# Performance work log

Measured on AMD Instinct MI355X. Metric: run time of the kernel, lower is better.

The kernel has to match this reference:

```python
import jax, jax.numpy as jnp
import numpy as np

B, P, NTIME, NLATENT, NSPATIAL = 4, 2, 16, 32, 2048


def sqrt_act(x):
    # signed square root: sign(x) * sqrt(|x|) (odd, monotone activation used in ERA5_PredRNN)
    return jnp.sign(x) * jnp.sqrt(jnp.abs(x))


def setup_inputs() -> dict:
    key = jax.random.key(0)
    ks = jax.random.split(key, 10)
    T, C, X = NTIME, NLATENT, NSPATIAL
    # xavier-uniform bounds (torch fan_in = T*C, fan_out = T*C for (t,T,c); T,T for 2D)
    s3 = (6.0 / (T * C + T * C)) ** 0.5
    s2 = (6.0 / (T + T)) ** 0.5
    x = jax.random.normal(ks[0], (B, P, T, C, X), jnp.float32)
    K0 = jax.random.uniform(ks[1], (T, T, C), jnp.float32, -s3, s3)
    Q0 = jax.random.uniform(ks[2], (T, T, C), jnp.float32, -s3, s3)
    V0 = jax.random.uniform(ks[3], (T, T, C), jnp.float32, -s3, s3)
    K1 = jax.random.uniform(ks[4], (T, T), jnp.float32, -s2, s2)
    Q1 = jax.random.uniform(ks[5], (T, T), jnp.float32, -s2, s2)
    V1 = jax.random.uniform(ks[6], (T, T), jnp.float32, -s2, s2)

    def ortho3(kk):
        # mimics nn.init.orthogonal_ on (T,T,T): rows (flattened to T x T*T) are orthonormal
        m = jax.random.normal(kk, (T * T, T), jnp.float32)
        q, _ = jnp.linalg.qr(m)  # (T*T, T), orthonormal columns
        return q.T.reshape(T, T, T)

    enc = ortho3(ks[7])
    dec = ortho3(ks[8])
    a = jnp.ones((T, X), jnp.float32)
    w = jnp.ones((T, X), jnp.float32) / (X * T)
    return dict(x=x, K0=K0, Q0=Q0, V0=V0, K1=K1, Q1=Q1, V1=V1,
                enc=enc, dec=dec, a=a, w=w)


def reference(x, K0, Q0, V0, K1, Q1, V1, enc, dec, a, w):
    # --- layer 0: per-latent-channel time mixing (tTc) ---
    k = jnp.einsum('tTc,bpTcx->bptcx', K0, x)
    q0 = jnp.einsum('tTc,bpTcx->bptcx', Q0, x)
    v = jnp.einsum('tTc,bpTcx->bptcx', V0, x)
    h = sqrt_act(jnp.einsum('bptcx,bpTcx,etT->bpecx', k, v, enc))
    # --- layer 1: shared time mixing (tT) ---
    k = jnp.einsum('tT,bpTcx->bptcx', K1, h)
    q1 = jnp.einsum('tT,bpTcx->bptcx', Q1, h)
    v = jnp.einsum('tT,bpTcx->bptcx', V1, h)
    h = sqrt_act(jnp.einsum('bptcx,bpTcx,etT->bpecx', k, v, enc))
    # estp: 'tx,bptcx->bptcx' (elementwise over t,x)
    b = a[None, None, :, None, :] * h
    # decoder mixing in reverse layer order (estb)
    b = jnp.einsum('bptcx,bpecx,etT->bpTcx', q1, b, dec)
    b = jnp.einsum('bptcx,bpecx,etT->bpTcx', q0, b, dec)
    # estc: 'tx,bptcx->bpc'
    y = jnp.einsum('tx,bptcx->bpc', w, b)
    return y[:, :, None, :]  # [B, p, 1, c]
```

## Files before the change

kernel.cpp:

```cpp
#include <hip/hip_runtime.h>
#include <math.h>

#define NB 4
#define NP 2
#define NT 16
#define NC 32
#define NX 2048


typedef _Float16 f16x8 __attribute__((ext_vector_type(8)));
typedef float f32x16 __attribute__((ext_vector_type(16)));

__device__ __forceinline__ unsigned short f16hi_bits(float v) {
    _Float16 h = (_Float16)v;
    return __builtin_bit_cast(unsigned short, h);
}
__device__ __forceinline__ unsigned short f16lo_bits(float v) {
    _Float16 h = (_Float16)v;
    _Float16 l = (_Float16)(v - (float)h);
    return __builtin_bit_cast(unsigned short, l);
}
__device__ __forceinline__ f16x8 frag_cast(uint4 u) {
    return __builtin_bit_cast(f16x8, u);
}
__device__ __forceinline__ float sqrt_act(float v) {
    const float s = __builtin_amdgcn_sqrtf(__builtin_fabsf(v));
    return copysignf(s, v);
}
__device__ __forceinline__ f32x16 zero16() {
    f32x16 z;
#pragma unroll
    for (int i = 0; i < 16; ++i) z[i] = 0.f;
    return z;
}

__device__ void g_compute(const float* __restrict__ K,
                          const float* __restrict__ V,
                          const float* __restrict__ enc,
                          int cstride, int c, int e, int tid,
                          float* sK, float* sV, float* sE, float* sW,
                          float* outG) {
    {
        const int t = tid >> 4, A = tid & 15;
        sK[tid] = K[(t * 16 + A) * cstride + c];
        sV[tid] = V[(t * 16 + A) * cstride + c];
        sE[tid] = enc[(e * 16 + t) * 16 + A];
    }
    __syncthreads();
    {
        const int t = tid >> 4, Bi = tid & 15;
        float acc = 0.f;
#pragma unroll
        for (int T = 0; T < 16; ++T) acc += sE[t * 16 + T] * sV[T * 16 + Bi];
        sW[tid] = acc;
    }
    __syncthreads();
    {
        const int A = tid >> 4, Bi = tid & 15;
        float acc = 0.f;
#pragma unroll
        for (int t = 0; t < 16; ++t) acc += sK[t * 16 + A] * sW[t * 16 + Bi];
        outG[tid] = acc;
    }
    __syncthreads();
}

__device__ void emit_half(const float* sG, uint4* __restrict__ dstPair,
                          int half, int tid) {
    if (tid < 64) {
        const int row = tid & 15, g = (tid >> 4) & 1, part = tid >> 5;
        unsigned dw[4];
#pragma unroll
        for (int d = 0; d < 4; ++d) {
            const float v0 = sG[row * 16 + g * 8 + 2 * d];
            const float v1 = sG[row * 16 + g * 8 + 2 * d + 1];
            const unsigned short s0 = part ? f16lo_bits(v0) : f16hi_bits(v0);
            const unsigned short s1 = part ? f16lo_bits(v1) : f16hi_bits(v1);
            dw[d] = (unsigned)s0 | ((unsigned)s1 << 16);
        }
        dstPair[part * 64 + g * 32 + 16 * half + row] =
            make_uint4(dw[0], dw[1], dw[2], dw[3]);
    }
}

__global__ __launch_bounds__(256) void precompute_all(
    const float* __restrict__ K0, const float* __restrict__ V0,
    const float* __restrict__ K1, const float* __restrict__ V1,
    const float* __restrict__ Q0, const float* __restrict__ Q1,
    const float* __restrict__ enc, const float* __restrict__ dec,
    uint4* __restrict__ AF0, uint4* __restrict__ AFG1,
    uint4* __restrict__ AFM1, uint4* __restrict__ AFM2,
    float* __restrict__ out) {
    __shared__ float sK[256], sV[256], sE[256], sW[256], sG[256];
    __shared__ float sDec[4096], sQ[256];
    const int b = blockIdx.x, tid = threadIdx.x;
    if (b < 512) {
        const int c = b >> 4, e = b & 15;
        g_compute(K0, V0, enc, NC, c, e, tid, sK, sV, sE, sW, sG);
        emit_half(sG, AF0 + (c * 8 + (e >> 1)) * 128, e & 1, tid);
    } else if (b < 528) {
        const int e = b - 512;
        g_compute(K1, V1, enc, 1, 0, e, tid, sK, sV, sE, sW, sG);
        emit_half(sG, AFG1 + (e >> 1) * 128, e & 1, tid);
    } else if (b < 536) {
        const int m = b - 528;
#pragma unroll
        for (int i = tid; i < 4096; i += 256) sDec[i] = dec[i];
        sQ[tid] = Q1[tid];
        __syncthreads();
        if (tid < 128) {
            const int part = tid >> 6, lane = tid & 63;
            const int row32 = lane & 31, g = lane >> 5;
            const int e = 2 * m + (row32 >> 4), E = row32 & 15;
            unsigned dw[4];
#pragma unroll
            for (int d = 0; d < 4; ++d) {
                unsigned short s01[2];
#pragma unroll
                for (int hh = 0; hh < 2; ++hh) {
                    const int T = g * 8 + 2 * d + hh;
                    float acc = 0.f;
#pragma unroll
                    for (int t = 0; t < 16; ++t)
                        acc += sQ[t * 16 + T] * sDec[(e * 16 + t) * 16 + E];
                    s01[hh] = part ? f16lo_bits(acc) : f16hi_bits(acc);
                }
                dw[d] = (unsigned)s01[0] | ((unsigned)s01[1] << 16);
            }
            AFM1[m * 128 + part * 64 + lane] = make_uint4(dw[0], dw[1], dw[2], dw[3]);
        }
    } else if (b < 792) {
        const int idx = b - 536;
        const int c = idx >> 3, m = idx & 7;
#pragma unroll
        for (int i = tid; i < 4096; i += 256) sDec[i] = dec[i];
        sQ[tid] = Q0[tid * NC + c];
        __syncthreads();
        if (tid < 128) {
            const int part = tid >> 6, lane = tid & 63;
            const int row32 = lane & 31, g = lane >> 5;
            const int T = 2 * m + (row32 >> 4), A = row32 & 15;
            unsigned dw[4];
#pragma unroll
            for (int d = 0; d < 4; ++d) {
                unsigned short s01[2];
#pragma unroll
                for (int hh = 0; hh < 2; ++hh) {
                    const int E = g * 8 + 2 * d + hh;
                    float acc = 0.f;
#pragma unroll
                    for (int t = 0; t < 16; ++t)
                        acc += sQ[t * 16 + A] * sDec[(E * 16 + t) * 16 + T];
                    s01[hh] = part ? f16lo_bits(acc) : f16hi_bits(acc);
                }
                dw[d] = (unsigned)s01[0] | ((unsigned)s01[1] << 16);
            }
            AFM2[(c * 8 + m) * 128 + part * 64 + lane] =
                make_uint4(dw[0], dw[1], dw[2], dw[3]);
        }
    } else {
        out[tid] = 0.f;
    }
}

__global__ __launch_bounds__(256) void site_kernel(
    const float* __restrict__ x,
    const float* __restrict__ a,
    const float* __restrict__ w,
    const uint4* __restrict__ AF0,
    const uint4* __restrict__ AFG1,
    const uint4* __restrict__ AFM1,
    const uint4* __restrict__ AFM2,
    float* __restrict__ out) {
    __shared__ float red[4];

    const int tid = threadIdx.x;
    const int lane = tid & 63, wid = tid >> 6;
    const int col = lane & 31, g = lane >> 5;
    const bool g0 = (g == 0);
    const int bid = blockIdx.x;
    const int xg = bid & 15;
    const int c  = (bid >> 4) & 31;
    const int bp = bid >> 9;
    const int xA = xg * 128 + wid * 32 + col;
    const float* xb = x + (bp * NT * NC + c) * NX;

    f16x8 Xh, Xl;
    float XC[8];
#pragma unroll
    for (int j = 0; j < 8; ++j) {
        const float v = xb[(g * 8 + j) * NC * NX + xA];
        const _Float16 hv = (_Float16)v;
        Xh[j] = hv; Xl[j] = (_Float16)(v - (float)hv);
    }
#pragma unroll
    for (int r = 0; r < 8; ++r) {
        const int A = (r & 3) + 8 * (r >> 2) + 4 * g;
        XC[r] = xb[A * NC * NX + xA];
    }

    const f32x16 Z0 = zero16();

    float h[16];
    {
        const uint4* p0 = AF0 + (c * 8) * 128 + lane;
#define S0_ITER(M)                                                          \
        do {                                                                \
            const f16x8 Ah = frag_cast(p0[(M) * 128]);                      \
            const f16x8 Al = frag_cast(p0[(M) * 128 + 64]);                 \
            f32x16 C = __builtin_amdgcn_mfma_f32_32x32x16_f16(Ah, Xh, Z0, 0, 0, 0); \
            C = __builtin_amdgcn_mfma_f32_32x32x16_f16(Ah, Xl, C, 0, 0, 0); \
            C = __builtin_amdgcn_mfma_f32_32x32x16_f16(Al, Xh, C, 0, 0, 0); \
            float se = 0.f, so = 0.f;                                       \
            _Pragma("unroll")                                               \
            for (int r = 0; r < 8; ++r) {                                   \
                se += XC[r] * C[r];                                         \
                so += XC[r] * C[r + 8];                                     \
            }                                                               \
            se += __shfl_xor(se, 32);                                       \
            so += __shfl_xor(so, 32);                                       \
            h[2 * (M)]     = sqrt_act(se);                                  \
            h[2 * (M) + 1] = sqrt_act(so);                                  \
        } while (0)
        S0_ITER(0); S0_ITER(1); S0_ITER(2); S0_ITER(3);
        S0_ITER(4); S0_ITER(5); S0_ITER(6); S0_ITER(7);
#undef S0_ITER
    }

    f16x8 hH, hL;
    float hC[8];
#define HPK(J)                                                              \
    {                                                                       \
        const float v = g0 ? h[J] : h[(J) + 8];              \
        const _Float16 hv = (_Float16)v;                                    \
        hH[J] = hv; hL[J] = (_Float16)(v - (float)hv);                      \
    }
    HPK(0) HPK(1) HPK(2) HPK(3) HPK(4) HPK(5) HPK(6) HPK(7)
#undef HPK
#define HCK(R, BASE) hC[R] = g0 ? h[BASE] : h[(BASE) + 4];
    HCK(0, 0) HCK(1, 1) HCK(2, 2) HCK(3, 3)
    HCK(4, 8) HCK(5, 9) HCK(6, 10) HCK(7, 11)
#undef HCK

    float b2[8];
#pragma unroll
    for (int r = 0; r < 8; ++r) b2[r] = 0.f;
    {
        const uint4* pG = AFG1 + lane;
        const uint4* pM = AFM1 + lane;
        const float* pa = a + xA;
#pragma unroll 1
        for (int m = 0; m < 8; ++m) {
            const f16x8 GH = frag_cast(pG[0]);
            const f16x8 GL = frag_cast(pG[64]);
            const f16x8 MH = frag_cast(pM[0]);
            const f16x8 ML = frag_cast(pM[64]);
            pG += 128; pM += 128;
            const float ae = pa[0], ao = pa[NX];
            pa += 2 * NX;
            f32x16 C = __builtin_amdgcn_mfma_f32_32x32x16_f16(GH, hH, Z0, 0, 0, 0);
            C = __builtin_amdgcn_mfma_f32_32x32x16_f16(GH, hL, C, 0, 0, 0);
            C = __builtin_amdgcn_mfma_f32_32x32x16_f16(GL, hH, C, 0, 0, 0);
            float se = 0.f, so = 0.f;
#pragma unroll
            for (int r = 0; r < 8; ++r) {
                se += hC[r] * C[r];
                so += hC[r] * C[r + 8];
            }
            se += __shfl_xor(se, 32);
            so += __shfl_xor(so, 32);
            const float pe = ae * sqrt_act(se);
            const float po = ao * sqrt_act(so);
            f32x16 U = __builtin_amdgcn_mfma_f32_32x32x16_f16(MH, hH, Z0, 0, 0, 0);
            U = __builtin_amdgcn_mfma_f32_32x32x16_f16(MH, hL, U, 0, 0, 0);
            U = __builtin_amdgcn_mfma_f32_32x32x16_f16(ML, hH, U, 0, 0, 0);
#pragma unroll
            for (int r = 0; r < 8; ++r)
                b2[r] += pe * U[r] + po * U[r + 8];
        }
    }

    f16x8 bH, bL;
#define BX(R)                                                               \
    {                                                                       \
        const float snd = g0 ? b2[(R) + 4] : b2[R];                         \
        const float rcv = __shfl_xor(snd, 32);                              \
        const float v0 = g0 ? b2[R] : rcv;             \
        const float v1 = g0 ? rcv : b2[(R) + 4];       \
        _Float16 hv = (_Float16)v0;                                         \
        bH[R] = hv;       bL[R]       = (_Float16)(v0 - (float)hv);         \
        hv = (_Float16)v1;                                                  \
        bH[(R) + 4] = hv; bL[(R) + 4] = (_Float16)(v1 - (float)hv);         \
    }
    BX(0) BX(1) BX(2) BX(3)
#undef BX

    float ya = 0.f;
    {
        const uint4* p2 = AFM2 + (c * 8) * 128 + lane;
        const float* pw = w + xA;
#pragma unroll 1
        for (int m = 0; m < 8; ++m) {
            const f16x8 MH = frag_cast(p2[0]);
            const f16x8 ML = frag_cast(p2[64]);
            p2 += 128;
            const float we = pw[0], wo = pw[NX];
            pw += 2 * NX;
            f32x16 Z = __builtin_amdgcn_mfma_f32_32x32x16_f16(MH, bH, Z0, 0, 0, 0);
            Z = __builtin_amdgcn_mfma_f32_32x32x16_f16(MH, bL, Z, 0, 0, 0);
            Z = __builtin_amdgcn_mfma_f32_32x32x16_f16(ML, bH, Z, 0, 0, 0);
            float se = 0.f, so = 0.f;
#pragma unroll
            for (int r = 0; r < 8; ++r) {
                se += XC[r] * Z[r];
                so += XC[r] * Z[r + 8];
            }
            ya += we * se + wo * so;
        }
    }

    float y = ya + __shfl_xor(ya, 32);
    y += __shfl_xor(y, 1); y += __shfl_xor(y, 2);
    y += __shfl_xor(y, 4); y += __shfl_xor(y, 8); y += __shfl_xor(y, 16);
    if (lane == 0) red[wid] = y;
    __syncthreads();
    if (tid == 0) {
        atomicAdd(&out[bp * NC + c], red[0] + red[1] + red[2] + red[3]);
    }
}

extern "C" void kernel_launch(void* const* d_in, const int* in_sizes, int n_in,
                              void* d_out, int out_size, void* d_ws, size_t ws_size,
                              hipStream_t stream) {
    const float* x   = (const float*)d_in[0];
    const float* K0  = (const float*)d_in[1];
    const float* Q0  = (const float*)d_in[2];
    const float* V0  = (const float*)d_in[3];
    const float* K1  = (const float*)d_in[4];
    const float* Q1  = (const float*)d_in[5];
    const float* V1  = (const float*)d_in[6];
    const float* enc = (const float*)d_in[7];
    const float* dec = (const float*)d_in[8];
    const float* a   = (const float*)d_in[9];
    const float* w   = (const float*)d_in[10];
    float* out = (float*)d_out;

    uint4* AF0  = (uint4*)d_ws;
    uint4* AFG1 = AF0  + 256 * 128;
    uint4* AFM1 = AFG1 + 8 * 128;
    uint4* AFM2 = AFM1 + 8 * 128;

    precompute_all<<<793, 256, 0, stream>>>(K0, V0, K1, V1, Q0, Q1,
                                            enc, dec, AF0, AFG1, AFM1, AFM2,
                                            out);

    const int nblocks = NB * NP * NC * (NX / 128);
    site_kernel<<<nblocks, 256, 0, stream>>>(x, a, w, AF0, AFG1, AFM1, AFM2, out);
}
```

Measured before the change: 163.1 us.

## Use single-wave blocks and prefetch MFMA weight fragments one step ahead

The site kernel now runs one 64-thread wavefront per block instead of four waves per block. This drops the shared-memory reduction and __syncthreads, at the cost of four times as many global atomicAdds into the output. All three MFMA stages now load the next iteration's A fragments before using the current ones, so global load latency can overlap with MFMA work. The prefetch reads one fragment past each stage's last one; those values are never used but may sit beyond the end of the AFM2 buffer.

```diff
diff --git a/kernel.cpp b/kernel.cpp
--- a/kernel.cpp
+++ b/kernel.cpp
@@ -163,7 +163,7 @@
     }
 }
 
-__global__ __launch_bounds__(256) void site_kernel(
+__global__ __launch_bounds__(64) void site_kernel(
     const float* __restrict__ x,
     const float* __restrict__ a,
     const float* __restrict__ w,
@@ -172,17 +172,14 @@
     const uint4* __restrict__ AFM1,
     const uint4* __restrict__ AFM2,
     float* __restrict__ out) {
-    __shared__ float red[4];
-
-    const int tid = threadIdx.x;
-    const int lane = tid & 63, wid = tid >> 6;
+    const int lane = threadIdx.x & 63;
     const int col = lane & 31, g = lane >> 5;
     const bool g0 = (g == 0);
     const int bid = blockIdx.x;
-    const int xg = bid & 15;
-    const int c  = (bid >> 4) & 31;
-    const int bp = bid >> 9;
-    const int xA = xg * 128 + wid * 32 + col;
+    const int xt = bid & 63;
+    const int c  = (bid >> 6) & 31;
+    const int bp = bid >> 11;
+    const int xA = xt * 32 + col;
     const float* xb = x + (bp * NT * NC + c) * NX;
 
     f16x8 Xh, Xl;
@@ -204,10 +201,13 @@
     float h[16];
     {
         const uint4* p0 = AF0 + (c * 8) * 128 + lane;
+        uint4 cAh = p0[0], cAl = p0[64];
 #define S0_ITER(M)                                                          \
         do {                                                                \
-            const f16x8 Ah = frag_cast(p0[(M) * 128]);                      \
-            const f16x8 Al = frag_cast(p0[(M) * 128 + 64]);                 \
+            const uint4 nAh = p0[((M) + 1) * 128];                          \
+            const uint4 nAl = p0[((M) + 1) * 128 + 64];                     \
+            const f16x8 Ah = frag_cast(cAh);                                \
+            const f16x8 Al = frag_cast(cAl);                                \
             f32x16 C = __builtin_amdgcn_mfma_f32_32x32x16_f16(Ah, Xh, Z0, 0, 0, 0); \
             C = __builtin_amdgcn_mfma_f32_32x32x16_f16(Ah, Xl, C, 0, 0, 0); \
             C = __builtin_amdgcn_mfma_f32_32x32x16_f16(Al, Xh, C, 0, 0, 0); \
@@ -221,6 +221,7 @@
             so += __shfl_xor(so, 32);                                       \
             h[2 * (M)]     = sqrt_act(se);                                  \
             h[2 * (M) + 1] = sqrt_act(so);                                  \
+            cAh = nAh; cAl = nAl;                                           \
         } while (0)
         S0_ITER(0); S0_ITER(1); S0_ITER(2); S0_ITER(3);
         S0_ITER(4); S0_ITER(5); S0_ITER(6); S0_ITER(7);
@@ -249,15 +250,18 @@
         const uint4* pG = AFG1 + lane;
         const uint4* pM = AFM1 + lane;
         const float* pa = a + xA;
+        uint4 cGH = pG[0], cGL = pG[64], cMH = pM[0], cML = pM[64];
 #pragma unroll 1
         for (int m = 0; m < 8; ++m) {
-            const f16x8 GH = frag_cast(pG[0]);
-            const f16x8 GL = frag_cast(pG[64]);
-            const f16x8 MH = frag_cast(pM[0]);
-            const f16x8 ML = frag_cast(pM[64]);
             pG += 128; pM += 128;
+            const uint4 nGH = pG[0], nGL = pG[64];
+            const uint4 nMH = pM[0], nML = pM[64];
             const float ae = pa[0], ao = pa[NX];
             pa += 2 * NX;
+            const f16x8 GH = frag_cast(cGH);
+            const f16x8 GL = frag_cast(cGL);
+            const f16x8 MH = frag_cast(cMH);
+            const f16x8 ML = frag_cast(cML);
             f32x16 C = __builtin_amdgcn_mfma_f32_32x32x16_f16(GH, hH, Z0, 0, 0, 0);
             C = __builtin_amdgcn_mfma_f32_32x32x16_f16(GH, hL, C, 0, 0, 0);
             C = __builtin_amdgcn_mfma_f32_32x32x16_f16(GL, hH, C, 0, 0, 0);
@@ -277,6 +281,7 @@
 #pragma unroll
             for (int r = 0; r < 8; ++r)
                 b2[r] += pe * U[r] + po * U[r + 8];
+            cGH = nGH; cGL = nGL; cMH = nMH; cML = nML;
         }
     }
 
@@ -299,13 +304,15 @@
     {
         const uint4* p2 = AFM2 + (c * 8) * 128 + lane;
         const float* pw = w + xA;
+        uint4 cMH = p2[0], cML = p2[64];
 #pragma unroll 1
         for (int m = 0; m < 8; ++m) {
-            const f16x8 MH = frag_cast(p2[0]);
-            const f16x8 ML = frag_cast(p2[64]);
             p2 += 128;
+            const uint4 nMH = p2[0], nML = p2[64];
             const float we = pw[0], wo = pw[NX];
             pw += 2 * NX;
+            const f16x8 MH = frag_cast(cMH);
+            const f16x8 ML = frag_cast(cML);
             f32x16 Z = __builtin_amdgcn_mfma_f32_32x32x16_f16(MH, bH, Z0, 0, 0, 0);
             Z = __builtin_amdgcn_mfma_f32_32x32x16_f16(MH, bL, Z, 0, 0, 0);
             Z = __builtin_amdgcn_mfma_f32_32x32x16_f16(ML, bH, Z, 0, 0, 0);
@@ -316,16 +323,15 @@
                 so += XC[r] * Z[r + 8];
             }
             ya += we * se + wo * so;
+            cMH = nMH; cML = nML;
         }
     }
 
     float y = ya + __shfl_xor(ya, 32);
     y += __shfl_xor(y, 1); y += __shfl_xor(y, 2);
     y += __shfl_xor(y, 4); y += __shfl_xor(y, 8); y += __shfl_xor(y, 16);
-    if (lane == 0) red[wid] = y;
-    __syncthreads();
-    if (tid == 0) {
-        atomicAdd(&out[bp * NC + c], red[0] + red[1] + red[2] + red[3]);
+    if (lane == 0) {
+        atomicAdd(&out[bp * NC + c], y);
     }
 }
 
@@ -354,6 +360,6 @@
                                             enc, dec, AF0, AFG1, AFM1, AFM2,
                                             out);
 
-    const int nblocks = NB * NP * NC * (NX / 128);
-    site_kernel<<<nblocks, 256, 0, stream>>>(x, a, w, AF0, AFG1, AFM1, AFM2, out);
-}
+    const int nblocks = NB * NP * NC * (NX / 32);
+    site_kernel<<<nblocks, 64, 0, stream>>>(x, a, w, AF0, AFG1, AFM1, AFM2, out);
+}
```

Measured after the change: 211.6 us. +29.7%, slower.
